# Performance work log

Hardware: AMD Instinct MI355X
Metric: run time of the kernel (lower is better)

Reference implementation:

```python
import jax, jax.numpy as jnp
import numpy as np

N = 50000      # nodes
E = 800000     # edges (before self loops)
IN = 256       # input feature dim
H = 4          # heads
C = 64         # hidden per head (concat=False -> mean over heads -> 64)
LAT = 32       # latent dim
ED = 3         # edge feature dim
NEG_SLOPE = 0.2


def setup_inputs() -> dict:
    key = jax.random.key(0)
    ks = jax.random.split(key, 24)
    nrm = lambda k, shp, s=0.05: jax.random.normal(k, shp, jnp.float32) * s
    inp = {
        'x': jax.random.normal(ks[0], (N, IN), jnp.float32),
        'edge_index': jax.random.randint(ks[1], (2, E), 0, N),
        'edge_attr': jax.random.normal(ks[2], (E, ED), jnp.float32),
    }
    i = 3
    for l, d in enumerate([IN, C]):  # layer 0 in_dim=IN, layer 1 in_dim=hidden
        inp[f'Wl{l}'] = nrm(ks[i], (d, H * C)); i += 1
        inp[f'bl{l}'] = jnp.zeros((H * C,), jnp.float32)
        inp[f'Wr{l}'] = nrm(ks[i], (d, H * C)); i += 1
        inp[f'br{l}'] = jnp.zeros((H * C,), jnp.float32)
        inp[f'We{l}'] = nrm(ks[i], (ED, H * C)); i += 1
        inp[f'att{l}'] = nrm(ks[i], (H, C)); i += 1
        inp[f'bias{l}'] = jnp.zeros((C,), jnp.float32)
    inp['Wmu'] = nrm(ks[i], (C, LAT)); i += 1
    inp['bmu'] = jnp.zeros((LAT,), jnp.float32)
    return inp


def _gatv2(x, edge_index, edge_attr, Wl, bl, Wr, br, We, att, bias):
    # PyG GATv2Conv: heads=H, concat=False, add_self_loops=True,
    # edge_dim=3, fill_value='mean', negative_slope=0.2, share_weights=False
    n = x.shape[0]
    src, dst = edge_index[0], edge_index[1]
    # self-loop edge_attr = mean of incoming edge_attr per node (0 if none)
    deg = jax.ops.segment_sum(jnp.ones((src.shape[0],), jnp.float32), dst, num_segments=n)
    loop_attr = jax.ops.segment_sum(edge_attr, dst, num_segments=n) / jnp.maximum(deg, 1.0)[:, None]
    loop = jnp.arange(n)
    s = jnp.concatenate([src, loop])
    d = jnp.concatenate([dst, loop])
    ea = jnp.concatenate([edge_attr, loop_attr], axis=0)
    xl = (x @ Wl + bl).reshape(n, H, C)   # source transform
    xr = (x @ Wr + br).reshape(n, H, C)   # target transform
    ee = (ea @ We).reshape(-1, H, C)      # edge transform (no bias)
    m = jax.nn.leaky_relu(xl[s] + xr[d] + ee, NEG_SLOPE)   # [Etot, H, C]
    alpha = jnp.einsum('ehc,hc->eh', m, att)                # [Etot, H]
    amax = jax.ops.segment_max(alpha, d, num_segments=n)    # per-dst max (all segments nonempty: self loops)
    ex = jnp.exp(alpha - amax[d])
    a = ex / jax.ops.segment_sum(ex, d, num_segments=n)[d]  # segment softmax
    out = jax.ops.segment_sum(xl[s] * a[:, :, None], d, num_segments=n)  # [N, H, C]
    return out.mean(axis=1) + bias  # concat=False -> head mean, then bias


def reference(x, edge_index, edge_attr,
              Wl0, bl0, Wr0, br0, We0, att0, bias0,
              Wl1, bl1, Wr1, br1, We1, att1, bias1,
              Wmu, bmu):
    h = jax.nn.relu(_gatv2(x, edge_index, edge_attr, Wl0, bl0, Wr0, br0, We0, att0, bias0))
    h = jax.nn.relu(_gatv2(h, edge_index, edge_attr, Wl1, bl1, Wr1, br1, We1, att1, bias1))
    return h @ Wmu + bmu
```

## Files before the change

### kernel.cpp

```cpp
#include <hip/hip_runtime.h>


#define NN  50000
#define EE  800000
#define HC  256
#define NSLOPE 0.2f
#define SCAN_B ((NN + 255) / 256)

typedef float f32x4 __attribute__((ext_vector_type(4)));
typedef short bf16x8 __attribute__((ext_vector_type(8)));

__device__ __forceinline__ unsigned short f2b(float f) {
    unsigned u = __float_as_uint(f);
    u += 0x7FFFu + ((u >> 16) & 1u);
    return (unsigned short)(u >> 16);
}
__device__ __forceinline__ float b2f(unsigned short h) {
    return __uint_as_float((unsigned)h << 16);
}

__global__ __launch_bounds__(256) void deg_kernel(
    const int* __restrict__ dst, int* __restrict__ deg)
{
    int i = blockIdx.x * 256 + threadIdx.x;
    if (i >= EE / 4) return;
    int4 v = ((const int4*)dst)[i];
    atomicAdd(&deg[v.x], 1);
    atomicAdd(&deg[v.y], 1);
    atomicAdd(&deg[v.z], 1);
    atomicAdd(&deg[v.w], 1);
}

__global__ __launch_bounds__(256) void scan1_kernel(
    const int* __restrict__ deg, int* __restrict__ rows, int* __restrict__ bsum)
{
    __shared__ int sh[256];
    const int t = threadIdx.x, b = blockIdx.x;
    const int i = b * 256 + t;
    int v = (i < NN) ? deg[i] : 0;
    sh[t] = v;
    __syncthreads();
    for (int off = 1; off < 256; off <<= 1) {
        int u = (t >= off) ? sh[t - off] : 0;
        __syncthreads();
        sh[t] += u;
        __syncthreads();
    }
    if (i < NN) rows[i] = sh[t] - v;
    if (t == 255) bsum[b] = sh[255];
}

__global__ __launch_bounds__(256) void scan2_kernel(int* __restrict__ bsum, int* __restrict__ boff)
{
    __shared__ int sh[256];
    const int t = threadIdx.x;
    int v = (t < SCAN_B) ? bsum[t] : 0;
    sh[t] = v;
    __syncthreads();
    for (int off = 1; off < 256; off <<= 1) {
        int u = (t >= off) ? sh[t - off] : 0;
        __syncthreads();
        sh[t] += u;
        __syncthreads();
    }
    if (t < SCAN_B) boff[t] = sh[t] - v;
}

__global__ __launch_bounds__(256) void scan3_kernel(
    int* __restrict__ rows, int* __restrict__ curs, const int* __restrict__ boff)
{
    const int b = blockIdx.x;
    const int i = b * 256 + threadIdx.x;
    if (i < NN) {
        int v = rows[i] + boff[b];
        rows[i] = v;
        curs[i] = v;
    }
    if (i == 0) rows[NN] = EE;
}

__global__ __launch_bounds__(256) void scatter_kernel(
    const int* __restrict__ ei, const float* __restrict__ ea,
    int* __restrict__ cursor, float4* __restrict__ csr)
{
    int i = blockIdx.x * 256 + threadIdx.x;
    if (i >= EE / 4) return;
    int4 s = ((const int4*)ei)[i];
    int4 d = ((const int4*)(ei + EE))[i];
    float4 e0 = ((const float4*)ea)[i * 3 + 0];
    float4 e1 = ((const float4*)ea)[i * 3 + 1];
    float4 e2 = ((const float4*)ea)[i * 3 + 2];
    int p0 = atomicAdd(&cursor[d.x], 1);
    int p1 = atomicAdd(&cursor[d.y], 1);
    int p2 = atomicAdd(&cursor[d.z], 1);
    int p3 = atomicAdd(&cursor[d.w], 1);
    csr[p0] = make_float4(__int_as_float(s.x), e0.x, e0.y, e0.z);
    csr[p1] = make_float4(__int_as_float(s.y), e0.w, e1.x, e1.y);
    csr[p2] = make_float4(__int_as_float(s.z), e1.z, e1.w, e2.x);
    csr[p3] = make_float4(__int_as_float(s.w), e2.y, e2.z, e2.w);
}

__global__ __launch_bounds__(256) void cvt_wt(
    const float* __restrict__ W, unsigned short* __restrict__ WTh,
    unsigned short* __restrict__ WTl, int K)
{
    int i = blockIdx.x * 256 + threadIdx.x;
    if (i >= K * 256) return;
    int k = i >> 8, c = i & 255;
    float v = W[i];
    unsigned short h = f2b(v);
    unsigned short l = f2b(v - b2f(h));
    WTh[(size_t)c * K + k] = h;
    WTl[(size_t)c * K + k] = l;
}

__global__ __launch_bounds__(256) void gemm_fused(
    const float* __restrict__ A,
    const unsigned short* __restrict__ BTh, const unsigned short* __restrict__ BTl,
    const float* __restrict__ bias0, const float* __restrict__ bias1,
    float* __restrict__ C0, float* __restrict__ C1,
    int M, int K)
{
    __shared__ unsigned short Ah[64][36], Al[64][36];
    __shared__ unsigned short Bh[256][36], Bl[256][36];
    const int tid = threadIdx.x;
    const int bm = blockIdx.y << 6;
    const int bn = blockIdx.x << 8;
    const int w  = tid >> 6, l = tid & 63;
    const int wr = w >> 1, wc = w & 1;
    const int lr = l & 15, lk = l >> 4;

    f32x4 acc[2][8];
#pragma unroll
    for (int a = 0; a < 2; a++)
#pragma unroll
        for (int b = 0; b < 8; b++) acc[a][b] = (f32x4){0.f, 0.f, 0.f, 0.f};

    const int ar = tid >> 2, ac = (tid & 3) << 3;

    for (int k0 = 0; k0 < K; k0 += 32) {
        float av[8];
        if (bm + ar < M) {
            *(float4*)&av[0] = *(const float4*)&A[(size_t)(bm + ar) * K + k0 + ac];
            *(float4*)&av[4] = *(const float4*)&A[(size_t)(bm + ar) * K + k0 + ac + 4];
        } else {
#pragma unroll
            for (int j = 0; j < 8; j++) av[j] = 0.f;
        }
        unsigned hp[4], lp[4];
#pragma unroll
        for (int j = 0; j < 4; j++) {
            unsigned short h0 = f2b(av[2 * j]),     h1 = f2b(av[2 * j + 1]);
            unsigned short l0 = f2b(av[2 * j]     - b2f(h0));
            unsigned short l1 = f2b(av[2 * j + 1] - b2f(h1));
            hp[j] = (unsigned)h0 | ((unsigned)h1 << 16);
            lp[j] = (unsigned)l0 | ((unsigned)l1 << 16);
        }
        *(uint4*)&Ah[ar][ac] = make_uint4(hp[0], hp[1], hp[2], hp[3]);
        *(uint4*)&Al[ar][ac] = make_uint4(lp[0], lp[1], lp[2], lp[3]);
#pragma unroll
        for (int rep = 0; rep < 4; rep++) {
            int i  = (rep << 8) + tid;
            int rb = i >> 2, cb = (i & 3) << 3;
            *(uint4*)&Bh[rb][cb] = *(const uint4*)&BTh[(size_t)(bn + rb) * K + k0 + cb];
            *(uint4*)&Bl[rb][cb] = *(const uint4*)&BTl[(size_t)(bn + rb) * K + k0 + cb];
        }
        __syncthreads();

        bf16x8 afh[2], afl[2];
#pragma unroll
        for (int a = 0; a < 2; a++) {
            afh[a] = *(const bf16x8*)&Ah[wr * 32 + a * 16 + lr][lk << 3];
            afl[a] = *(const bf16x8*)&Al[wr * 32 + a * 16 + lr][lk << 3];
        }
#pragma unroll
        for (int b = 0; b < 8; b++) {
            bf16x8 bh  = *(const bf16x8*)&Bh[wc * 128 + b * 16 + lr][lk << 3];
            bf16x8 bl_ = *(const bf16x8*)&Bl[wc * 128 + b * 16 + lr][lk << 3];
#pragma unroll
            for (int a = 0; a < 2; a++) {
                acc[a][b] = __builtin_amdgcn_mfma_f32_16x16x32_bf16(afh[a], bh,  acc[a][b], 0, 0, 0);
                acc[a][b] = __builtin_amdgcn_mfma_f32_16x16x32_bf16(afh[a], bl_, acc[a][b], 0, 0, 0);
                acc[a][b] = __builtin_amdgcn_mfma_f32_16x16x32_bf16(afl[a], bh,  acc[a][b], 0, 0, 0);
            }
        }
        __syncthreads();
    }

    const float* bias = (bn == 0) ? bias0 : bias1;
    float* C = (bn == 0) ? C0 : C1;
#pragma unroll
    for (int a = 0; a < 2; a++) {
        int rbase = bm + wr * 32 + a * 16 + (lk << 2);
#pragma unroll
        for (int b = 0; b < 8; b++) {
            int c = wc * 128 + b * 16 + lr;
            float bs = bias[c];
#pragma unroll
            for (int i = 0; i < 4; i++) {
                int rg = rbase + i;
                if (rg < M) C[(size_t)rg * HC + c] = acc[a][b][i] + bs;
            }
        }
    }
}

__global__ __launch_bounds__(256) void gat_edge(
    const float* __restrict__ xl, const float* __restrict__ xr,
    const float4* __restrict__ csr, const int* __restrict__ row_start,
    const float* __restrict__ att, const float* __restrict__ We,
    const float* __restrict__ bias, float* __restrict__ out)
{
    const int lane = threadIdx.x & 63;
    const int node = (blockIdx.x * 256 + threadIdx.x) >> 6;
    if (node >= NN) return;
    const int j4 = lane << 2;
    const float4* xlv = (const float4*)xl;

    const float4 xr4 = *(const float4*)&xr[(size_t)node * HC + j4];
    const float4 at4 = *(const float4*)&att[j4];
    const float4 w0  = *(const float4*)&We[j4];
    const float4 w1  = *(const float4*)&We[HC + j4];
    const float4 w2  = *(const float4*)&We[2 * HC + j4];

    float acc0 = 0.f, acc1 = 0.f, acc2 = 0.f, acc3 = 0.f, denom = 0.f;
    float eas0 = 0.f, eas1 = 0.f, eas2 = 0.f;
    const int beg = row_start[node];
    const int n   = row_start[node + 1] - beg;
    const float4* cp = csr + beg;

    float4 r0 = {0,0,0,0}, r1 = {0,0,0,0}, r2 = {0,0,0,0};
    float4 v0 = {0,0,0,0}, v1 = {0,0,0,0};
    if (n > 0) { r0 = cp[0]; v0 = xlv[(unsigned)(__float_as_int(r0.x) * 64 + lane)]; }
    if (n > 1) { r1 = cp[1]; v1 = xlv[(unsigned)(__float_as_int(r1.x) * 64 + lane)]; }
    if (n > 2) { r2 = cp[2]; }

    for (int i = 0; i < n; i++) {
        float4 crec = r0, cxv = v0;
        r0 = r1; r1 = r2; v0 = v1;
        if (i + 3 < n) r2 = cp[i + 3];
        if (i + 2 < n) v1 = xlv[(unsigned)(__float_as_int(r1.x) * 64 + lane)];

        float ea0 = crec.y, ea1 = crec.z, ea2 = crec.w;
        eas0 += ea0; eas1 += ea1; eas2 += ea2;
        float m0 = cxv.x + xr4.x + ea0 * w0.x + ea1 * w1.x + ea2 * w2.x;
        float m1 = cxv.y + xr4.y + ea0 * w0.y + ea1 * w1.y + ea2 * w2.y;
        float m2 = cxv.z + xr4.z + ea0 * w0.z + ea1 * w1.z + ea2 * w2.z;
        float m3 = cxv.w + xr4.w + ea0 * w0.w + ea1 * w1.w + ea2 * w2.w;
        m0 = fmaxf(m0, NSLOPE * m0);
        m1 = fmaxf(m1, NSLOPE * m1);
        m2 = fmaxf(m2, NSLOPE * m2);
        m3 = fmaxf(m3, NSLOPE * m3);
        float p = m0 * at4.x + m1 * at4.y + m2 * at4.z + m3 * at4.w;
        p += __shfl_xor(p, 1);
        p += __shfl_xor(p, 2);
        p += __shfl_xor(p, 4);
        p += __shfl_xor(p, 8);
        float ex = __expf(p);
        denom += ex;
        acc0 = fmaf(ex, cxv.x, acc0);
        acc1 = fmaf(ex, cxv.y, acc1);
        acc2 = fmaf(ex, cxv.z, acc2);
        acc3 = fmaf(ex, cxv.w, acc3);
    }

    {
        float rd = 1.0f / fmaxf((float)n, 1.0f);
        float ea0 = eas0 * rd, ea1 = eas1 * rd, ea2 = eas2 * rd;
        float4 sv = xlv[(unsigned)(node * 64 + lane)];
        float m0 = sv.x + xr4.x + ea0 * w0.x + ea1 * w1.x + ea2 * w2.x;
        float m1 = sv.y + xr4.y + ea0 * w0.y + ea1 * w1.y + ea2 * w2.y;
        float m2 = sv.z + xr4.z + ea0 * w0.z + ea1 * w1.z + ea2 * w2.z;
        float m3 = sv.w + xr4.w + ea0 * w0.w + ea1 * w1.w + ea2 * w2.w;
        m0 = fmaxf(m0, NSLOPE * m0);
        m1 = fmaxf(m1, NSLOPE * m1);
        m2 = fmaxf(m2, NSLOPE * m2);
        m3 = fmaxf(m3, NSLOPE * m3);
        float p = m0 * at4.x + m1 * at4.y + m2 * at4.z + m3 * at4.w;
        p += __shfl_xor(p, 1);
        p += __shfl_xor(p, 2);
        p += __shfl_xor(p, 4);
        p += __shfl_xor(p, 8);
        float ex = __expf(p);
        denom += ex;
        acc0 = fmaf(ex, sv.x, acc0);
        acc1 = fmaf(ex, sv.y, acc1);
        acc2 = fmaf(ex, sv.z, acc2);
        acc3 = fmaf(ex, sv.w, acc3);
    }

    const float inv = 1.0f / denom;
    float r0s = acc0 * inv, r1s = acc1 * inv, r2s = acc2 * inv, r3s = acc3 * inv;
    r0s += __shfl_xor(r0s, 16); r0s += __shfl_xor(r0s, 32);
    r1s += __shfl_xor(r1s, 16); r1s += __shfl_xor(r1s, 32);
    r2s += __shfl_xor(r2s, 16); r2s += __shfl_xor(r2s, 32);
    r3s += __shfl_xor(r3s, 16); r3s += __shfl_xor(r3s, 32);
    if (lane < 16) {
        float4 bv = *(const float4*)&bias[j4];
        float4 o;
        o.x = fmaxf(0.25f * r0s + bv.x, 0.f);
        o.y = fmaxf(0.25f * r1s + bv.y, 0.f);
        o.z = fmaxf(0.25f * r2s + bv.z, 0.f);
        o.w = fmaxf(0.25f * r3s + bv.w, 0.f);
        *(float4*)&out[(size_t)node * 64 + j4] = o;
    }
}

__global__ __launch_bounds__(256) void mu_kernel(
    const float* __restrict__ h, const float* __restrict__ Wmu,
    const float* __restrict__ bmu, float* __restrict__ out)
{
    __shared__ float ws[64 * 32];
    __shared__ float hs[8 * 64];
    const int tid = threadIdx.x;
#pragma unroll
    for (int i = 0; i < 8; i++) ws[tid + i * 256] = Wmu[tid + i * 256];
    const int nb = blockIdx.x * 8;
    {
        int idx = tid * 2;
        *(float2*)&hs[idx] = *(const float2*)&h[(size_t)nb * 64 + idx];
    }
    __syncthreads();
    const int ln = tid >> 5;
    const int o  = tid & 31;
    float acc = bmu[o];
#pragma unroll
    for (int k = 0; k < 64; k++) acc = fmaf(hs[ln * 64 + k], ws[k * 32 + o], acc);
    out[(size_t)(nb + ln) * 32 + o] = acc;
}

extern "C" void kernel_launch(void* const* d_in, const int* in_sizes, int n_in,
                              void* d_out, int out_size, void* d_ws, size_t ws_size,
                              hipStream_t stream) {
    const float* x    = (const float*)d_in[0];
    const int*   ei   = (const int*)  d_in[1];
    const float* ea   = (const float*)d_in[2];
    const float* Wl0  = (const float*)d_in[3];
    const float* bl0  = (const float*)d_in[4];
    const float* Wr0  = (const float*)d_in[5];
    const float* br0  = (const float*)d_in[6];
    const float* We0  = (const float*)d_in[7];
    const float* att0 = (const float*)d_in[8];
    const float* bi0  = (const float*)d_in[9];
    const float* Wl1  = (const float*)d_in[10];
    const float* bl1  = (const float*)d_in[11];
    const float* Wr1  = (const float*)d_in[12];
    const float* br1  = (const float*)d_in[13];
    const float* We1  = (const float*)d_in[14];
    const float* att1 = (const float*)d_in[15];
    const float* bi1  = (const float*)d_in[16];
    const float* Wmu  = (const float*)d_in[17];
    const float* bmu  = (const float*)d_in[18];
    float* out = (float*)d_out;

    float* xl32 = (float*)d_ws;
    float* xr32 = xl32 + (size_t)NN * HC;
    float* h1   = xr32 + (size_t)NN * HC;
    int*   deg  = (int*)(h1 + (size_t)NN * 64);
    int*   rows = deg + NN;
    int*   curs = rows + NN + 1;
    int*   bsum = curs + NN;
    int*   boff = bsum + SCAN_B;
    uintptr_t p = (uintptr_t)(boff + SCAN_B);
    p = (p + 15) & ~(uintptr_t)15;
    unsigned short* WT0h = (unsigned short*)p;
    unsigned short* WT0l = WT0h + 512 * 256;
    unsigned short* WT1h = WT0l + 512 * 256;
    unsigned short* WT1l = WT1h + 512 * 64;
    p = (uintptr_t)(WT1l + 512 * 64);
    p = (p + 255) & ~(uintptr_t)255;
    float4* csr = (float4*)p;

    hipMemsetAsync(deg, 0, NN * sizeof(int), stream);
    deg_kernel<<<(EE / 4 + 255) / 256, 256, 0, stream>>>(ei + EE, deg);
    scan1_kernel<<<SCAN_B, 256, 0, stream>>>(deg, rows, bsum);
    scan2_kernel<<<1, 256, 0, stream>>>(bsum, boff);
    scan3_kernel<<<SCAN_B, 256, 0, stream>>>(rows, curs, boff);
    scatter_kernel<<<(EE / 4 + 255) / 256, 256, 0, stream>>>(ei, ea, curs, csr);

    cvt_wt<<<256, 256, 0, stream>>>(Wl0, WT0h,             WT0l,             256);
    cvt_wt<<<256, 256, 0, stream>>>(Wr0, WT0h + 256 * 256, WT0l + 256 * 256, 256);
    cvt_wt<<< 64, 256, 0, stream>>>(Wl1, WT1h,             WT1l,             64);
    cvt_wt<<< 64, 256, 0, stream>>>(Wr1, WT1h + 256 * 64,  WT1l + 256 * 64,  64);

    dim3 gg(2, (NN + 63) / 64);
    const int gat_grid = (NN * 64) / 256;

    gemm_fused<<<gg, 256, 0, stream>>>(x, WT0h, WT0l, bl0, br0, xl32, xr32, NN, 256);
    gat_edge<<<gat_grid, 256, 0, stream>>>(xl32, xr32, csr, rows, att0, We0, bi0, h1);

    gemm_fused<<<gg, 256, 0, stream>>>(h1, WT1h, WT1l, bl1, br1, xl32, xr32, NN, 64);
    gat_edge<<<gat_grid, 256, 0, stream>>>(xl32, xr32, csr, rows, att1, We1, bi1, h1);

    mu_kernel<<<NN / 8, 256, 0, stream>>>(h1, Wmu, bmu, out);
}
```

Before: 598.7 us.

## Fuse CSR build and weight conversion into one cooperative kernel; fuse mu projection into second GAT

Replaces the memset, degree count, three scan kernels, scatter and four weight-conversion launches with a single cooperative kernel that uses grid-wide syncs between phases. Edge data is loaded into registers before the first sync and reused for the scatter. The final 64->32 linear projection is folded into the second gat_edge launch through a template flag, so h1 is never written and re-read. The goal is fewer launches and less intermediate traffic. In exchange, every block must be co-resident for the cooperative launch, and the grid syncs plus the per-block staging of Wmu in shared memory add overhead.

```diff
diff --git a/kernel.cpp b/kernel.cpp
--- a/kernel.cpp
+++ b/kernel.cpp
@@ -1,4 +1,5 @@
 #include <hip/hip_runtime.h>
+#include <hip/hip_cooperative_groups.h>
 
 
 #define NN  50000
@@ -6,6 +7,9 @@
 #define HC  256
 #define NSLOPE 0.2f
 #define SCAN_B ((NN + 255) / 256)
+#define NB_BUILD ((EE / 4 + 255) / 256)
+
+namespace cg = cooperative_groups;
 
 typedef float f32x4 __attribute__((ext_vector_type(4)));
 typedef short bf16x8 __attribute__((ext_vector_type(8)));
@@ -19,99 +23,114 @@
     return __uint_as_float((unsigned)h << 16);
 }
 
-__global__ __launch_bounds__(256) void deg_kernel(
-    const int* __restrict__ dst, int* __restrict__ deg)
+struct BuildParams {
+    const int* ei; const float* ea;
+    int* deg; int* rows; int* curs; int* bsum; int* boff;
+    float4* csr;
+    const float* Wl0; const float* Wr0; const float* Wl1; const float* Wr1;
+    unsigned short* WT0h; unsigned short* WT0l;
+    unsigned short* WT1h; unsigned short* WT1l;
+};
+
+__global__ __launch_bounds__(256) void build_kernel(BuildParams P)
 {
-    int i = blockIdx.x * 256 + threadIdx.x;
-    if (i >= EE / 4) return;
-    int4 v = ((const int4*)dst)[i];
-    atomicAdd(&deg[v.x], 1);
-    atomicAdd(&deg[v.y], 1);
-    atomicAdd(&deg[v.z], 1);
-    atomicAdd(&deg[v.w], 1);
-}
-
-__global__ __launch_bounds__(256) void scan1_kernel(
-    const int* __restrict__ deg, int* __restrict__ rows, int* __restrict__ bsum)
-{
+    cg::grid_group grid = cg::this_grid();
+    const int tid = threadIdx.x;
+    const int gid = blockIdx.x * 256 + tid;
+    const int gsz = gridDim.x * 256;
     __shared__ int sh[256];
-    const int t = threadIdx.x, b = blockIdx.x;
-    const int i = b * 256 + t;
-    int v = (i < NN) ? deg[i] : 0;
-    sh[t] = v;
-    __syncthreads();
-    for (int off = 1; off < 256; off <<= 1) {
-        int u = (t >= off) ? sh[t - off] : 0;
+
+    for (int i = gid; i < NN; i += gsz) P.deg[i] = 0;
+    for (int i = gid; i < 256 * 256; i += gsz) {
+        int k = i >> 8, c = i & 255;
+        float v = P.Wl0[i];
+        unsigned short h = f2b(v);
+        P.WT0h[c * 256 + k] = h; P.WT0l[c * 256 + k] = f2b(v - b2f(h));
+        v = P.Wr0[i];
+        h = f2b(v);
+        P.WT0h[(256 + c) * 256 + k] = h; P.WT0l[(256 + c) * 256 + k] = f2b(v - b2f(h));
+    }
+    for (int i = gid; i < 64 * 256; i += gsz) {
+        int k = i >> 8, c = i & 255;
+        float v = P.Wl1[i];
+        unsigned short h = f2b(v);
+        P.WT1h[c * 64 + k] = h; P.WT1l[c * 64 + k] = f2b(v - b2f(h));
+        v = P.Wr1[i];
+        h = f2b(v);
+        P.WT1h[(256 + c) * 64 + k] = h; P.WT1l[(256 + c) * 64 + k] = f2b(v - b2f(h));
+    }
+    const int ii = gid;
+    const bool ev = ii < EE / 4;
+    int4 s4 = {0, 0, 0, 0}, d4 = {0, 0, 0, 0};
+    float4 e0 = {0, 0, 0, 0}, e1 = {0, 0, 0, 0}, e2 = {0, 0, 0, 0};
+    if (ev) {
+        s4 = ((const int4*)P.ei)[ii];
+        d4 = ((const int4*)(P.ei + EE))[ii];
+        e0 = ((const float4*)P.ea)[ii * 3 + 0];
+        e1 = ((const float4*)P.ea)[ii * 3 + 1];
+        e2 = ((const float4*)P.ea)[ii * 3 + 2];
+    }
+    grid.sync();
+
+    if (ev) {
+        atomicAdd(&P.deg[d4.x], 1);
+        atomicAdd(&P.deg[d4.y], 1);
+        atomicAdd(&P.deg[d4.z], 1);
+        atomicAdd(&P.deg[d4.w], 1);
+    }
+    grid.sync();
+
+    if (blockIdx.x < SCAN_B) {
+        int i = blockIdx.x * 256 + tid;
+        int v = (i < NN) ? P.deg[i] : 0;
+        sh[tid] = v;
         __syncthreads();
-        sh[t] += u;
+        for (int off = 1; off < 256; off <<= 1) {
+            int u = (tid >= off) ? sh[tid - off] : 0;
+            __syncthreads();
+            sh[tid] += u;
+            __syncthreads();
+        }
+        if (i < NN) P.rows[i] = sh[tid] - v;
+        if (tid == 255) P.bsum[blockIdx.x] = sh[255];
+    }
+    grid.sync();
+
+    if (blockIdx.x == 0) {
+        int v = (tid < SCAN_B) ? P.bsum[tid] : 0;
+        sh[tid] = v;
         __syncthreads();
-    }
-    if (i < NN) rows[i] = sh[t] - v;
-    if (t == 255) bsum[b] = sh[255];
-}
-
-__global__ __launch_bounds__(256) void scan2_kernel(int* __restrict__ bsum, int* __restrict__ boff)
-{
-    __shared__ int sh[256];
-    const int t = threadIdx.x;
-    int v = (t < SCAN_B) ? bsum[t] : 0;
-    sh[t] = v;
-    __syncthreads();
-    for (int off = 1; off < 256; off <<= 1) {
-        int u = (t >= off) ? sh[t - off] : 0;
-        __syncthreads();
-        sh[t] += u;
-        __syncthreads();
-    }
-    if (t < SCAN_B) boff[t] = sh[t] - v;
-}
-
-__global__ __launch_bounds__(256) void scan3_kernel(
-    int* __restrict__ rows, int* __restrict__ curs, const int* __restrict__ boff)
-{
-    const int b = blockIdx.x;
-    const int i = b * 256 + threadIdx.x;
-    if (i < NN) {
-        int v = rows[i] + boff[b];
-        rows[i] = v;
-        curs[i] = v;
-    }
-    if (i == 0) rows[NN] = EE;
-}
-
-__global__ __launch_bounds__(256) void scatter_kernel(
-    const int* __restrict__ ei, const float* __restrict__ ea,
-    int* __restrict__ cursor, float4* __restrict__ csr)
-{
-    int i = blockIdx.x * 256 + threadIdx.x;
-    if (i >= EE / 4) return;
-    int4 s = ((const int4*)ei)[i];
-    int4 d = ((const int4*)(ei + EE))[i];
-    float4 e0 = ((const float4*)ea)[i * 3 + 0];
-    float4 e1 = ((const float4*)ea)[i * 3 + 1];
-    float4 e2 = ((const float4*)ea)[i * 3 + 2];
-    int p0 = atomicAdd(&cursor[d.x], 1);
-    int p1 = atomicAdd(&cursor[d.y], 1);
-    int p2 = atomicAdd(&cursor[d.z], 1);
-    int p3 = atomicAdd(&cursor[d.w], 1);
-    csr[p0] = make_float4(__int_as_float(s.x), e0.x, e0.y, e0.z);
-    csr[p1] = make_float4(__int_as_float(s.y), e0.w, e1.x, e1.y);
-    csr[p2] = make_float4(__int_as_float(s.z), e1.z, e1.w, e2.x);
-    csr[p3] = make_float4(__int_as_float(s.w), e2.y, e2.z, e2.w);
-}
-
-__global__ __launch_bounds__(256) void cvt_wt(
-    const float* __restrict__ W, unsigned short* __restrict__ WTh,
-    unsigned short* __restrict__ WTl, int K)
-{
-    int i = blockIdx.x * 256 + threadIdx.x;
-    if (i >= K * 256) return;
-    int k = i >> 8, c = i & 255;
-    float v = W[i];
-    unsigned short h = f2b(v);
-    unsigned short l = f2b(v - b2f(h));
-    WTh[(size_t)c * K + k] = h;
-    WTl[(size_t)c * K + k] = l;
+        for (int off = 1; off < 256; off <<= 1) {
+            int u = (tid >= off) ? sh[tid - off] : 0;
+            __syncthreads();
+            sh[tid] += u;
+            __syncthreads();
+        }
+        if (tid < SCAN_B) P.boff[tid] = sh[tid] - v;
+    }
+    grid.sync();
+
+    if (blockIdx.x < SCAN_B) {
+        int i = blockIdx.x * 256 + tid;
+        if (i < NN) {
+            int v = P.rows[i] + P.boff[blockIdx.x];
+            P.rows[i] = v;
+            P.curs[i] = v;
+        }
+    }
+    if (gid == 0) P.rows[NN] = EE;
+    grid.sync();
+
+    if (ev) {
+        int p0 = atomicAdd(&P.curs[d4.x], 1);
+        int p1 = atomicAdd(&P.curs[d4.y], 1);
+        int p2 = atomicAdd(&P.curs[d4.z], 1);
+        int p3 = atomicAdd(&P.curs[d4.w], 1);
+        P.csr[p0] = make_float4(__int_as_float(s4.x), e0.x, e0.y, e0.z);
+        P.csr[p1] = make_float4(__int_as_float(s4.y), e0.w, e1.x, e1.y);
+        P.csr[p2] = make_float4(__int_as_float(s4.z), e1.z, e1.w, e2.x);
+        P.csr[p3] = make_float4(__int_as_float(s4.w), e2.y, e2.z, e2.w);
+    }
 }
 
 __global__ __launch_bounds__(256) void gemm_fused(
@@ -205,15 +224,17 @@
     }
 }
 
+template<int FUSE>
 __global__ __launch_bounds__(256) void gat_edge(
     const float* __restrict__ xl, const float* __restrict__ xr,
     const float4* __restrict__ csr, const int* __restrict__ row_start,
     const float* __restrict__ att, const float* __restrict__ We,
-    const float* __restrict__ bias, float* __restrict__ out)
+    const float* __restrict__ bias, float* __restrict__ out,
+    const float* __restrict__ Wmu, const float* __restrict__ bmu,
+    float* __restrict__ mu_out)
 {
     const int lane = threadIdx.x & 63;
     const int node = (blockIdx.x * 256 + threadIdx.x) >> 6;
-    if (node >= NN) return;
     const int j4 = lane << 2;
     const float4* xlv = (const float4*)xl;
 
@@ -295,38 +316,42 @@
     r1s += __shfl_xor(r1s, 16); r1s += __shfl_xor(r1s, 32);
     r2s += __shfl_xor(r2s, 16); r2s += __shfl_xor(r2s, 32);
     r3s += __shfl_xor(r3s, 16); r3s += __shfl_xor(r3s, 32);
-    if (lane < 16) {
-        float4 bv = *(const float4*)&bias[j4];
-        float4 o;
-        o.x = fmaxf(0.25f * r0s + bv.x, 0.f);
-        o.y = fmaxf(0.25f * r1s + bv.y, 0.f);
-        o.z = fmaxf(0.25f * r2s + bv.z, 0.f);
-        o.w = fmaxf(0.25f * r3s + bv.w, 0.f);
-        *(float4*)&out[(size_t)node * 64 + j4] = o;
-    }
-}
-
-__global__ __launch_bounds__(256) void mu_kernel(
-    const float* __restrict__ h, const float* __restrict__ Wmu,
-    const float* __restrict__ bmu, float* __restrict__ out)
-{
-    __shared__ float ws[64 * 32];
-    __shared__ float hs[8 * 64];
-    const int tid = threadIdx.x;
-#pragma unroll
-    for (int i = 0; i < 8; i++) ws[tid + i * 256] = Wmu[tid + i * 256];
-    const int nb = blockIdx.x * 8;
-    {
-        int idx = tid * 2;
-        *(float2*)&hs[idx] = *(const float2*)&h[(size_t)nb * 64 + idx];
-    }
-    __syncthreads();
-    const int ln = tid >> 5;
-    const int o  = tid & 31;
-    float acc = bmu[o];
-#pragma unroll
-    for (int k = 0; k < 64; k++) acc = fmaf(hs[ln * 64 + k], ws[k * 32 + o], acc);
-    out[(size_t)(nb + ln) * 32 + o] = acc;
+
+    if (FUSE) {
+        __shared__ float WmuS[64 * 32];
+        __shared__ float bmuS[32];
+        __shared__ float hsh[4][64];
+        const int w = threadIdx.x >> 6;
+        if (lane < 16) {
+            float4 bv = *(const float4*)&bias[j4];
+            float* hp = &hsh[w][j4];
+            hp[0] = fmaxf(0.25f * r0s + bv.x, 0.f);
+            hp[1] = fmaxf(0.25f * r1s + bv.y, 0.f);
+            hp[2] = fmaxf(0.25f * r2s + bv.z, 0.f);
+            hp[3] = fmaxf(0.25f * r3s + bv.w, 0.f);
+        }
+        for (int i = threadIdx.x; i < 2048; i += 256) WmuS[i] = Wmu[i];
+        if (threadIdx.x < 32) bmuS[threadIdx.x] = bmu[threadIdx.x];
+        __syncthreads();
+        const int o  = lane & 31;
+        const int kh = (lane >> 5) << 5;
+        float accm = 0.f;
+#pragma unroll
+        for (int k = 0; k < 32; k++)
+            accm = fmaf(hsh[w][kh + k], WmuS[(kh + k) * 32 + o], accm);
+        accm += __shfl_xor(accm, 32);
+        if (lane < 32) mu_out[(size_t)node * 32 + o] = accm + bmuS[o];
+    } else {
+        if (lane < 16) {
+            float4 bv = *(const float4*)&bias[j4];
+            float4 oo;
+            oo.x = fmaxf(0.25f * r0s + bv.x, 0.f);
+            oo.y = fmaxf(0.25f * r1s + bv.y, 0.f);
+            oo.z = fmaxf(0.25f * r2s + bv.z, 0.f);
+            oo.w = fmaxf(0.25f * r3s + bv.w, 0.f);
+            *(float4*)&out[(size_t)node * 64 + j4] = oo;
+        }
+    }
 }
 
 extern "C" void kernel_launch(void* const* d_in, const int* in_sizes, int n_in,
@@ -371,26 +396,24 @@
     p = (p + 255) & ~(uintptr_t)255;
     float4* csr = (float4*)p;
 
-    hipMemsetAsync(deg, 0, NN * sizeof(int), stream);
-    deg_kernel<<<(EE / 4 + 255) / 256, 256, 0, stream>>>(ei + EE, deg);
-    scan1_kernel<<<SCAN_B, 256, 0, stream>>>(deg, rows, bsum);
-    scan2_kernel<<<1, 256, 0, stream>>>(bsum, boff);
-    scan3_kernel<<<SCAN_B, 256, 0, stream>>>(rows, curs, boff);
-    scatter_kernel<<<(EE / 4 + 255) / 256, 256, 0, stream>>>(ei, ea, curs, csr);
-
-    cvt_wt<<<256, 256, 0, stream>>>(Wl0, WT0h,             WT0l,             256);
-    cvt_wt<<<256, 256, 0, stream>>>(Wr0, WT0h + 256 * 256, WT0l + 256 * 256, 256);
-    cvt_wt<<< 64, 256, 0, stream>>>(Wl1, WT1h,             WT1l,             64);
-    cvt_wt<<< 64, 256, 0, stream>>>(Wr1, WT1h + 256 * 64,  WT1l + 256 * 64,  64);
+    BuildParams bp;
+    bp.ei = ei;   bp.ea = ea;
+    bp.deg = deg; bp.rows = rows; bp.curs = curs; bp.bsum = bsum; bp.boff = boff;
+    bp.csr = csr;
+    bp.Wl0 = Wl0; bp.Wr0 = Wr0; bp.Wl1 = Wl1; bp.Wr1 = Wr1;
+    bp.WT0h = WT0h; bp.WT0l = WT0l; bp.WT1h = WT1h; bp.WT1l = WT1l;
+    void* kargs[] = { &bp };
+    hipLaunchCooperativeKernel((const void*)build_kernel,
+                               dim3(NB_BUILD), dim3(256), kargs, 0, stream);
 
     dim3 gg(2, (NN + 63) / 64);
     const int gat_grid = (NN * 64) / 256;
 
     gemm_fused<<<gg, 256, 0, stream>>>(x, WT0h, WT0l, bl0, br0, xl32, xr32, NN, 256);
-    gat_edge<<<gat_grid, 256, 0, stream>>>(xl32, xr32, csr, rows, att0, We0, bi0, h1);
+    gat_edge<0><<<gat_grid, 256, 0, stream>>>(xl32, xr32, csr, rows, att0, We0, bi0, h1,
+                                              nullptr, nullptr, nullptr);
 
     gemm_fused<<<gg, 256, 0, stream>>>(h1, WT1h, WT1l, bl1, br1, xl32, xr32, NN, 64);
-    gat_edge<<<gat_grid, 256, 0, stream>>>(xl32, xr32, csr, rows, att1, We1, bi1, h1);
-
-    mu_kernel<<<NN / 8, 256, 0, stream>>>(h1, Wmu, bmu, out);
-}
+    gat_edge<1><<<gat_grid, 256, 0, stream>>>(xl32, xr32, csr, rows, att1, We1, bi1, nullptr,
+                                              Wmu, bmu, out);
+}
```

Result: slower. 1.044 ms (+74.4%).
